# Kernel optimization log

Measured on AMD Instinct MI355X. Metric: run time of the kernel, lower is better.

The kernel has to match this reference:

```python
import jax, jax.numpy as jnp
import numpy as np

# --- APPM / NMS pipeline constants (3 ratio groups on the 28x28 mixed feature map) ---
RATIOS = [4, 6, 8]            # square sliding-window sizes in feature cells
N_LIST = [2, 3, 2]            # proposals kept per group (proposalN = 7)
IOU_THRESHS = [0.25, 0.25, 0.25]
FM_SIZE = 28                  # mixed feature map spatial size
STRIDE = 16                   # 448 / 28: feature cell -> image pixels
IMG = 448
PROPOSAL_N = sum(N_LIST)
GROUP_SIZES = [(FM_SIZE - r + 1) ** 2 for r in RATIOS]


def make_coordinates():
    """[x0, y0, x1, y1] image-space boxes for every sliding window, all groups concatenated."""
    coords = []
    for r in RATIOS:
        n = FM_SIZE - r + 1
        ii, jj = np.meshgrid(np.arange(n), np.arange(n), indexing='ij')
        x0 = (ii.ravel() * STRIDE).astype(np.int32)
        y0 = (jj.ravel() * STRIDE).astype(np.int32)
        coords.append(np.stack([x0, y0, x0 + r * STRIDE, y0 + r * STRIDE], axis=1))
    return np.concatenate(coords, axis=0).astype(np.int32)   # (1595, 4)


def window_scores_from_fm(fm):
    """AvgPool2d(r, stride=1) then sum over channels == reduce_window over channel-summed map."""
    s = jnp.sum(fm, axis=1)  # (B, H, W)
    outs = []
    for r in RATIOS:
        w = jax.lax.reduce_window(s, 0.0, jax.lax.add, (1, r, r), (1, 1, 1), 'VALID') / float(r * r)
        outs.append(w.reshape(s.shape[0], -1))
    return jnp.concatenate(outs, axis=1)  # (B, sum(GROUP_SIZES))


def nms_group(scores, boxes, n_sel, thresh):
    """Greedy IoU NMS, exactly the inclusive (+1) box math of the source nms()."""
    areas = (boxes[:, 2] - boxes[:, 0] + 1.0) * (boxes[:, 3] - boxes[:, 1] + 1.0)

    def body(k, carry):
        sc, idxs = carry
        i = jnp.argmax(sc)                       # highest remaining score
        idxs = idxs.at[k].set(i.astype(jnp.int32))
        b = boxes[i]
        xx0 = jnp.maximum(boxes[:, 0], b[0]); yy0 = jnp.maximum(boxes[:, 1], b[1])
        xx1 = jnp.minimum(boxes[:, 2], b[2]); yy1 = jnp.minimum(boxes[:, 3], b[3])
        w = xx1 - xx0 + 1.0; h = yy1 - yy0 + 1.0
        inter = jnp.where((w < 0) | (h < 0), 0.0, w * h)
        iou = inter / (areas + areas[i] - inter)
        sc = jnp.where(iou > thresh, -jnp.inf, sc)  # suppress (selected box has iou=1 -> removed)
        return sc, idxs

    _, idxs = jax.lax.fori_loop(0, n_sel, body, (scores, jnp.zeros((n_sel,), jnp.int32)))
    return idxs


def select_proposals(all_scores, coordinates):
    parts = []
    off = 0
    for ng, n_sel, th in zip(GROUP_SIZES, N_LIST, IOU_THRESHS):
        sc = all_scores[:, off:off + ng]
        bx = coordinates[off:off + ng].astype(jnp.float32)
        idx = jax.vmap(lambda s: nms_group(s, bx, n_sel, th))(sc) + off
        parts.append(idx)
        off += ng
    return jnp.concatenate(parts, axis=1)  # (B, PROPOSAL_N) global window indices


def crop_windows(x, coordinates, indices):
    """Gather-crop each proposal window from the raw image, bilinear-resize to 448x448."""
    outs = []
    col = 0
    for r, n_sel in zip(RATIOS, N_LIST):
        w = r * STRIDE  # fixed crop size for this ratio group
        idx_g = indices[:, col:col + n_sel]

        def crop_one(img, gi):
            c = coordinates[gi]
            patch = jax.lax.dynamic_slice(img, (0, c[0], c[1]), (3, w, w))
            return jax.image.resize(patch, (3, IMG, IMG), 'bilinear')

        crops = jax.vmap(lambda img, gis: jax.vmap(lambda gi: crop_one(img, gi))(gis))(x, idx_g)
        outs.append(crops)
        col += n_sel
    return jnp.concatenate(outs, axis=1)  # (B, PROPOSAL_N, 3, 448, 448)


def setup_inputs() -> dict:
    key = jax.random.key(0)
    k1, k2, k3, k4 = jax.random.split(key, 4)
    B = 8
    return {
        'x': jax.random.normal(k1, (B, 3, IMG, IMG), jnp.float32),
        'fm': jax.random.normal(k2, (B, 384, FM_SIZE, FM_SIZE), jnp.float32),
        'embedding': jax.random.normal(k3, (B, 2048), jnp.float32),
        'W_cls': jax.random.normal(k4, (2048, 200), jnp.float32) * 0.02,
        'b_cls': jnp.zeros((200,), jnp.float32),
        'coordinates': jnp.asarray(make_coordinates()),
    }


def reference(x, fm, embedding, W_cls, b_cls, coordinates):
    all_scores = window_scores_from_fm(fm)                              # window_scores (B, 1595)
    proposalN_indices = select_proposals(all_scores, coordinates)       # (B, 7) int32
    proposalN_windows_scores = jnp.take_along_axis(all_scores, proposalN_indices, axis=1)
    window_imgs = crop_windows(x, coordinates, proposalN_indices)
    window_imgs = window_imgs.reshape(-1, 3, IMG, IMG)                  # (B*7, 3, 448, 448)
    raw_logits = embedding @ W_cls + b_cls                              # rawcls_net
    return (proposalN_indices, proposalN_windows_scores, all_scores, window_imgs, raw_logits)
```

## Files before the change

kernel.cpp:

```cpp
#include <hip/hip_runtime.h>
#include <math.h>

#define THREADS 256

typedef float f32x4 __attribute__((ext_vector_type(4)));

__global__ __launch_bounds__(THREADS) void fused1_kernel(const float* __restrict__ fm,
                                                         float4* __restrict__ part,
                                                         int cpc, int K,
                                                         const float* __restrict__ emb,
                                                         const float* __restrict__ W,
                                                         float* __restrict__ lpart) {
    int blk = blockIdx.x;
    int t = threadIdx.x;
    if (blk < 8 * K) {
        int b = blk / K, k = blk - b * K;
        if (t >= 196) return;
        const float4* f = (const float4*)(fm + ((size_t)b * 384 + (size_t)k * cpc) * 784);
        float4 acc = {0.0f, 0.0f, 0.0f, 0.0f};
        for (int c = 0; c < cpc; ++c) {
            float4 v = f[(size_t)c * 196 + t];
            acc.x += v.x; acc.y += v.y; acc.z += v.z; acc.w += v.w;
        }
        part[((size_t)b * K + k) * 196 + t] = acc;
    } else {
        int idx = blk - 8 * K;
        int b = idx >> 4, kc = idx & 15;
        if (t >= 200) return;
        const float* e  = emb + (size_t)b * 2048 + kc * 128;
        const float* wp = W + (size_t)kc * 128 * 200 + t;
        float acc = 0.0f;
        #pragma unroll 4
        for (int k = 0; k < 128; ++k)
            acc += e[k] * wp[(size_t)k * 200];
        lpart[((size_t)b * 16 + kc) * 200 + t] = acc;
    }
}

__global__ __launch_bounds__(THREADS) void fused2_kernel(const float4* __restrict__ part,
                                                         int K,
                                                         float* __restrict__ all_scores,
                                                         float* __restrict__ out_idx_f,
                                                         float* __restrict__ out_sc,
                                                         int* __restrict__ ws_idx,
                                                         const float* __restrict__ lpart,
                                                         const float* __restrict__ bias,
                                                         float* __restrict__ logits) {
    __shared__ float4 s4[196];
    __shared__ float  pref[28][29];
    __shared__ float  scl[625];
    __shared__ float  rv[4];
    __shared__ int    ri[4];
    int t = threadIdx.x;

    if (blockIdx.x >= 24) {
        int b = blockIdx.x - 24;
        if (t >= 200) return;
        float acc = bias[t];
        #pragma unroll
        for (int kc = 0; kc < 16; ++kc)
            acc += lpart[((size_t)b * 16 + kc) * 200 + t];
        logits[b * 200 + t] = acc;
        return;
    }

    int b = blockIdx.x / 3, g = blockIdx.x - b * 3;

    if (t < 196) {
        float4 acc = {0.0f, 0.0f, 0.0f, 0.0f};
        #pragma unroll 8
        for (int k = 0; k < K; ++k) {
            float4 v = part[((size_t)b * K + k) * 196 + t];
            acc.x += v.x; acc.y += v.y; acc.z += v.z; acc.w += v.w;
        }
        s4[t] = acc;
    }
    __syncthreads();
    if (t < 28) {
        float4 row[7];
        #pragma unroll
        for (int i = 0; i < 7; ++i) row[i] = s4[t * 7 + i];
        float run = 0.0f;
        pref[t][0] = 0.0f;
        #pragma unroll
        for (int j = 0; j < 28; ++j) {
            run += ((float*)row)[j];
            pref[t][j + 1] = run;
        }
    }
    __syncthreads();

    const int gnA[3]   = {625, 529, 441};
    const int sideA[3] = {25, 23, 21};
    const int rA[3]    = {4, 6, 8};
    const int nselA[3] = {2, 3, 2};
    const int colA[3]  = {0, 2, 5};
    const int goffA[3] = {0, 625, 1154};

    int n = gnA[g], side = sideA[g], r = rA[g];
    int nsel = nselA[g], goff = goffA[g], colbase = colA[g];
    float inv = 1.0f / (float)(r * r);

    for (int loc = t; loc < n; loc += THREADS) {
        int i = loc / side, j = loc % side;
        float acc = 0.0f;
        for (int a = 0; a < r; ++a)
            acc += pref[i + a][j + r] - pref[i + a][j];
        float sv = acc * inv;
        scl[loc] = sv;
        all_scores[b * 1595 + goff + loc] = sv;
    }
    __syncthreads();

    float ext = (float)(r * 16 + 1);
    float A   = ext * ext;
    float rs  = (float)(r * 16);

    for (int k = 0; k < nsel; ++k) {
        float bv = -INFINITY; int bi = 0x7fffffff;
        for (int i = t; i < n; i += THREADS) {
            float v = scl[i];
            if (v > bv || (v == bv && i < bi)) { bv = v; bi = i; }
        }
        #pragma unroll
        for (int m = 1; m < 64; m <<= 1) {
            float ov = __shfl_xor(bv, m, 64);
            int   oi = __shfl_xor(bi, m, 64);
            if (ov > bv || (ov == bv && oi < bi)) { bv = ov; bi = oi; }
        }
        int wv = t >> 6;
        if ((t & 63) == 0) { rv[wv] = bv; ri[wv] = bi; }
        __syncthreads();
        if (t == 0) {
            for (int q = 1; q < 4; ++q) {
                float ov = rv[q]; int oi = ri[q];
                if (ov > bv || (ov == bv && oi < bi)) { bv = ov; bi = oi; }
            }
            ri[0] = bi;
            int outp = b * 7 + colbase + k;
            out_idx_f[outp] = (float)(goff + bi);
            out_sc[outp]    = bv;
            ws_idx[outp]    = goff + bi;
        }
        __syncthreads();
        int sel = ri[0];
        int si = sel / side, sj = sel % side;
        float sx0 = si * 16.0f, sy0 = sj * 16.0f;
        float sx1 = sx0 + rs,   sy1 = sy0 + rs;
        for (int i = t; i < n; i += THREADS) {
            int ii = i / side, jj = i % side;
            float x0 = ii * 16.0f, y0 = jj * 16.0f;
            float x1 = x0 + rs,    y1 = y0 + rs;
            float xx0 = fmaxf(x0, sx0), yy0 = fmaxf(y0, sy0);
            float xx1 = fminf(x1, sx1), yy1 = fminf(y1, sy1);
            float w = xx1 - xx0 + 1.0f, h = yy1 - yy0 + 1.0f;
            float inter = (w < 0.0f || h < 0.0f) ? 0.0f : w * h;
            float iou = inter / (A + A - inter);
            if (iou > 0.25f) scl[i] = -INFINITY;
        }
        __syncthreads();
    }
}

#define CROP_GRID 1024
#define NTASK (56 * 3 * 28)

__global__ __launch_bounds__(448) void crop_kernel(const float* __restrict__ x,
                                                   const int* __restrict__ coords,
                                                   const int* __restrict__ ws_idx,
                                                   float* __restrict__ out) {
    __shared__ float lds[2][7 * 132];
    int t = threadIdx.x;

    int rr0 = t / 132,        xx0 = t - rr0 * 132;
    int i1  = t + 448;
    int rr1 = i1 / 132,       xx1 = i1 - rr1 * 132;
    int rr2 = 6,              xx2 = t + 104;
    int row_sub = t / 56;
    int seg     = t - row_sub * 56;
    int ox0 = seg * 8;

    int task = blockIdx.x;

    int    c_w, c_rlo, c_S;
    float  c_scale, c_wm1;
    size_t c_outb;
    const float* c_base;
    float rA, rB, rC;

    {
        int p = task / 84, rem = task - p * 84;
        int ch = rem / 28, stripe = rem - ch * 28;
        int b = p / 7, col = p - b * 7;
        int g = (col < 2) ? 0 : ((col < 5) ? 1 : 2);
        c_w = (g == 0) ? 64 : ((g == 1) ? 96 : 128);
        c_scale = (float)c_w * (1.0f / 448.0f);
        c_wm1 = (float)(c_w - 1);
        c_S = stripe * 16;
        float syb = fminf(fmaxf(((float)c_S + 0.5f) * c_scale - 0.5f, 0.0f), c_wm1);
        c_rlo = (int)syb;
        int gi = ws_idx[p];
        int c0 = coords[gi * 4 + 0];
        int c1 = coords[gi * 4 + 1];
        c_base = x + (((size_t)b * 3 + ch) * 448) * 448 + c1 + (size_t)c0 * 448;
        c_outb = (((size_t)p * 3 + ch) * 448) * 448;
        rA = c_base[(size_t)min(c_rlo + rr0, c_w - 1) * 448 + min(xx0, c_w - 1)];
        rB = c_base[(size_t)min(c_rlo + rr1, c_w - 1) * 448 + min(xx1, c_w - 1)];
        if (t < 28)
            rC = c_base[(size_t)min(c_rlo + rr2, c_w - 1) * 448 + min(xx2, c_w - 1)];
    }

    int buf = 0;
    while (true) {
        lds[buf][t]       = rA;
        lds[buf][t + 448] = rB;
        if (t < 28) lds[buf][t + 896] = rC;

        int nxt = task + CROP_GRID;
        bool has_nxt = nxt < NTASK;
        int    n_w = 0, n_rlo = 0, n_S = 0;
        float  n_scale = 0.0f, n_wm1 = 0.0f;
        size_t n_outb = 0;
        const float* n_base = nullptr;
        float nA = 0.0f, nB = 0.0f, nC = 0.0f;
        if (has_nxt) {
            int p = nxt / 84, rem = nxt - p * 84;
            int ch = rem / 28, stripe = rem - ch * 28;
            int b = p / 7, col = p - b * 7;
            int g = (col < 2) ? 0 : ((col < 5) ? 1 : 2);
            n_w = (g == 0) ? 64 : ((g == 1) ? 96 : 128);
            n_scale = (float)n_w * (1.0f / 448.0f);
            n_wm1 = (float)(n_w - 1);
            n_S = stripe * 16;
            float syb = fminf(fmaxf(((float)n_S + 0.5f) * n_scale - 0.5f, 0.0f), n_wm1);
            n_rlo = (int)syb;
            int gi = ws_idx[p];
            int c0 = coords[gi * 4 + 0];
            int c1 = coords[gi * 4 + 1];
            n_base = x + (((size_t)b * 3 + ch) * 448) * 448 + c1 + (size_t)c0 * 448;
            n_outb = (((size_t)p * 3 + ch) * 448) * 448;
            nA = n_base[(size_t)min(n_rlo + rr0, n_w - 1) * 448 + min(xx0, n_w - 1)];
            nB = n_base[(size_t)min(n_rlo + rr1, n_w - 1) * 448 + min(xx1, n_w - 1)];
            if (t < 28)
                nC = n_base[(size_t)min(n_rlo + rr2, n_w - 1) * 448 + min(xx2, n_w - 1)];
        }

        __syncthreads();

        {
            float sxb = ((float)ox0 + 0.5f) * c_scale - 0.5f;
            float sxc = fminf(fmaxf(sxb, 0.0f), c_wm1);
            int   i0  = (int)sxc;
            int   dk[8];
            float txk[8];
            #pragma unroll
            for (int k = 0; k < 8; ++k) {
                float sx = fminf(fmaxf(sxb + (float)k * c_scale, 0.0f), c_wm1);
                int xi = (int)sx;
                dk[k]  = xi - i0;
                txk[k] = sx - (float)xi;
            }
            const float* lbase = &lds[buf][0];
            #pragma unroll
            for (int half = 0; half < 2; ++half) {
                int oy = c_S + half * 8 + row_sub;
                float sy = fminf(fmaxf(((float)oy + 0.5f) * c_scale - 0.5f, 0.0f), c_wm1);
                int   y0 = (int)sy;
                int   y1 = min(y0 + 1, c_w - 1);
                float ty = sy - (float)y0;
                const float* l0 = lbase + (y0 - c_rlo) * 132 + i0;
                const float* l1 = lbase + (y1 - c_rlo) * 132 + i0;
                float a0 = l0[0], a1 = l0[1], a2 = l0[2], a3 = l0[3];
                float b0 = l1[0], b1 = l1[1], b2 = l1[2], b3 = l1[3];

                f32x4 res0, res1;
                #pragma unroll
                for (int k = 0; k < 8; ++k) {
                    int   d   = dk[k];
                    float v00 = (d == 0) ? a0 : ((d == 1) ? a1 : a2);
                    float v01 = (d == 0) ? a1 : ((d == 1) ? a2 : a3);
                    float v10 = (d == 0) ? b0 : ((d == 1) ? b1 : b2);
                    float v11 = (d == 0) ? b1 : ((d == 1) ? b2 : b3);
                    float tx  = txk[k];
                    float top = v00 + tx * (v01 - v00);
                    float bot = v10 + tx * (v11 - v10);
                    float rr  = top + ty * (bot - top);
                    if (k < 4) res0[k] = rr; else res1[k - 4] = rr;
                }
                float* orow = out + c_outb + (size_t)oy * 448 + ox0;
                *(f32x4*)orow       = res0;
                *(f32x4*)(orow + 4) = res1;
            }
        }

        if (!has_nxt) break;
        c_w = n_w; c_rlo = n_rlo; c_S = n_S;
        c_scale = n_scale; c_wm1 = n_wm1;
        c_outb = n_outb; c_base = n_base;
        rA = nA; rB = nB; rC = nC;
        task = nxt;
        buf ^= 1;
    }
}

extern "C" void kernel_launch(void* const* d_in, const int* in_sizes, int n_in,
                              void* d_out, int out_size, void* d_ws, size_t ws_size,
                              hipStream_t stream) {
    const float* x      = (const float*)d_in[0];
    const float* fm     = (const float*)d_in[1];
    const float* emb    = (const float*)d_in[2];
    const float* Wc     = (const float*)d_in[3];
    const float* bc     = (const float*)d_in[4];
    const int*   coords = (const int*)d_in[5];

    float* out        = (float*)d_out;
    float* out_idx    = out;
    float* out_sc     = out + 56;
    float* all_scores = out + 112;
    float* imgs       = out + 12872;
    float* logits     = out + 33731144;

    int K = 32;
    while (K > 1 && ws_size < 1024 + (size_t)8 * K * 784 * 4 + 25600 * 4) K >>= 1;
    int cpc = 384 / K;

    int*    ws_idx = (int*)d_ws;
    float4* part   = (float4*)((char*)d_ws + 1024);
    float*  lpart  = (float*)((char*)d_ws + 1024 + (size_t)8 * K * 784 * 4);

    fused1_kernel<<<8 * K + 128, THREADS, 0, stream>>>(fm, part, cpc, K, emb, Wc, lpart);
    fused2_kernel<<<32, THREADS, 0, stream>>>(part, K, all_scores, out_idx, out_sc, ws_idx,
                                              lpart, bc, logits);
    crop_kernel<<<CROP_GRID, 448, 0, stream>>>(x, coords, ws_idx, imgs);
}
```

Measured before the change: 53.12 us.

## Precompute crop source offsets and overlap next-task loads with resize compute

The selection kernel now writes a per-proposal pixel offset into the source image, so the crop kernel no longer does a dependent ws_idx→coords lookup chain. In the crop loop, the LDS store and a lightweight barrier come before the next task's global loads, which are issued after the barrier so they are in flight during the current bilinear compute. The interpolation select is rewritten as precomputed differences plus fmaf, and the persistent grid changes from 1024 to 944 blocks. The main risks are correctness of the hand-written barrier ordering and uneven load balance from the new grid size.

```diff
diff --git a/kernel.cpp b/kernel.cpp
--- a/kernel.cpp
+++ b/kernel.cpp
@@ -2,6 +2,8 @@
 #include <math.h>
 
 #define THREADS 256
+#define CROP_GRID 944
+#define NTASK (56 * 3 * 28)
 
 typedef float f32x4 __attribute__((ext_vector_type(4)));
 
@@ -43,6 +45,8 @@
                                                          float* __restrict__ out_idx_f,
                                                          float* __restrict__ out_sc,
                                                          int* __restrict__ ws_idx,
+                                                         int* __restrict__ soff,
+                                                         const int* __restrict__ coords,
                                                          const float* __restrict__ lpart,
                                                          const float* __restrict__ bias,
                                                          float* __restrict__ logits) {
@@ -138,9 +142,11 @@
             }
             ri[0] = bi;
             int outp = b * 7 + colbase + k;
-            out_idx_f[outp] = (float)(goff + bi);
+            int gi   = goff + bi;
+            out_idx_f[outp] = (float)gi;
             out_sc[outp]    = bv;
-            ws_idx[outp]    = goff + bi;
+            ws_idx[outp]    = gi;
+            soff[outp]      = coords[gi * 4 + 0] * 448 + coords[gi * 4 + 1];
         }
         __syncthreads();
         int sel = ri[0];
@@ -162,142 +168,131 @@
     }
 }
 
-#define CROP_GRID 1024
-#define NTASK (56 * 3 * 28)
-
 __global__ __launch_bounds__(448) void crop_kernel(const float* __restrict__ x,
-                                                   const int* __restrict__ coords,
-                                                   const int* __restrict__ ws_idx,
+                                                   const int* __restrict__ soff,
                                                    float* __restrict__ out) {
-    __shared__ float lds[2][7 * 132];
+    __shared__ float lds[2][924];
     int t = threadIdx.x;
 
-    int rr0 = t / 132,        xx0 = t - rr0 * 132;
+    int rr0 = t / 132, xx0 = t - rr0 * 132;
     int i1  = t + 448;
-    int rr1 = i1 / 132,       xx1 = i1 - rr1 * 132;
-    int rr2 = 6,              xx2 = t + 104;
+    int rr1 = i1 / 132, xx1 = i1 - rr1 * 132;
+    int xx2 = t + 104;
     int row_sub = t / 56;
     int seg     = t - row_sub * 56;
     int ox0 = seg * 8;
 
     int task = blockIdx.x;
-
-    int    c_w, c_rlo, c_S;
-    float  c_scale, c_wm1;
-    size_t c_outb;
-    const float* c_base;
-    float rA, rB, rC;
-
+    int cw; float cscale, cwm1; int cS, crlo; float* coutb;
+    float rA, rB, rC = 0.0f;
     {
         int p = task / 84, rem = task - p * 84;
         int ch = rem / 28, stripe = rem - ch * 28;
         int b = p / 7, col = p - b * 7;
         int g = (col < 2) ? 0 : ((col < 5) ? 1 : 2);
-        c_w = (g == 0) ? 64 : ((g == 1) ? 96 : 128);
-        c_scale = (float)c_w * (1.0f / 448.0f);
-        c_wm1 = (float)(c_w - 1);
-        c_S = stripe * 16;
-        float syb = fminf(fmaxf(((float)c_S + 0.5f) * c_scale - 0.5f, 0.0f), c_wm1);
-        c_rlo = (int)syb;
-        int gi = ws_idx[p];
-        int c0 = coords[gi * 4 + 0];
-        int c1 = coords[gi * 4 + 1];
-        c_base = x + (((size_t)b * 3 + ch) * 448) * 448 + c1 + (size_t)c0 * 448;
-        c_outb = (((size_t)p * 3 + ch) * 448) * 448;
-        rA = c_base[(size_t)min(c_rlo + rr0, c_w - 1) * 448 + min(xx0, c_w - 1)];
-        rB = c_base[(size_t)min(c_rlo + rr1, c_w - 1) * 448 + min(xx1, c_w - 1)];
+        cw = (g == 0) ? 64 : ((g == 1) ? 96 : 128);
+        cscale = (float)cw * (1.0f / 448.0f);
+        cwm1 = (float)(cw - 1);
+        cS = stripe * 16;
+        float syb = fminf(fmaxf(((float)cS + 0.5f) * cscale - 0.5f, 0.0f), cwm1);
+        crlo = (int)syb;
+        const float* cbase = x + ((size_t)(b * 3 + ch)) * 200704 + soff[p];
+        coutb = out + ((size_t)(p * 3 + ch)) * 200704;
+        rA = cbase[(size_t)min(crlo + rr0, cw - 1) * 448 + min(xx0, cw - 1)];
+        rB = cbase[(size_t)min(crlo + rr1, cw - 1) * 448 + min(xx1, cw - 1)];
         if (t < 28)
-            rC = c_base[(size_t)min(c_rlo + rr2, c_w - 1) * 448 + min(xx2, c_w - 1)];
+            rC = cbase[(size_t)min(crlo + 6, cw - 1) * 448 + min(xx2, cw - 1)];
     }
 
     int buf = 0;
     while (true) {
-        lds[buf][t]       = rA;
-        lds[buf][t + 448] = rB;
-        if (t < 28) lds[buf][t + 896] = rC;
-
         int nxt = task + CROP_GRID;
-        bool has_nxt = nxt < NTASK;
-        int    n_w = 0, n_rlo = 0, n_S = 0;
-        float  n_scale = 0.0f, n_wm1 = 0.0f;
-        size_t n_outb = 0;
-        const float* n_base = nullptr;
-        float nA = 0.0f, nB = 0.0f, nC = 0.0f;
-        if (has_nxt) {
+        bool has = nxt < NTASK;
+
+        int nw = 0, nrlo = 0, nS = 0, nso = 0, nb3 = 0, np3 = 0;
+        float nscale = 0.0f, nwm1 = 0.0f;
+        if (has) {
             int p = nxt / 84, rem = nxt - p * 84;
             int ch = rem / 28, stripe = rem - ch * 28;
             int b = p / 7, col = p - b * 7;
             int g = (col < 2) ? 0 : ((col < 5) ? 1 : 2);
-            n_w = (g == 0) ? 64 : ((g == 1) ? 96 : 128);
-            n_scale = (float)n_w * (1.0f / 448.0f);
-            n_wm1 = (float)(n_w - 1);
-            n_S = stripe * 16;
-            float syb = fminf(fmaxf(((float)n_S + 0.5f) * n_scale - 0.5f, 0.0f), n_wm1);
-            n_rlo = (int)syb;
-            int gi = ws_idx[p];
-            int c0 = coords[gi * 4 + 0];
-            int c1 = coords[gi * 4 + 1];
-            n_base = x + (((size_t)b * 3 + ch) * 448) * 448 + c1 + (size_t)c0 * 448;
-            n_outb = (((size_t)p * 3 + ch) * 448) * 448;
-            nA = n_base[(size_t)min(n_rlo + rr0, n_w - 1) * 448 + min(xx0, n_w - 1)];
-            nB = n_base[(size_t)min(n_rlo + rr1, n_w - 1) * 448 + min(xx1, n_w - 1)];
+            nw = (g == 0) ? 64 : ((g == 1) ? 96 : 128);
+            nscale = (float)nw * (1.0f / 448.0f);
+            nwm1 = (float)(nw - 1);
+            nS = stripe * 16;
+            float syb = fminf(fmaxf(((float)nS + 0.5f) * nscale - 0.5f, 0.0f), nwm1);
+            nrlo = (int)syb;
+            nso = soff[p];
+            nb3 = b * 3 + ch;
+            np3 = p * 3 + ch;
+        }
+
+        lds[buf][t]       = rA;
+        lds[buf][t + 448] = rB;
+        if (t < 28) lds[buf][t + 896] = rC;
+        asm volatile("s_waitcnt lgkmcnt(0)" ::: "memory");
+        __builtin_amdgcn_s_barrier();
+
+        float* noutb = nullptr;
+        if (has) {
+            const float* nbase = x + (size_t)nb3 * 200704 + nso;
+            noutb = out + (size_t)np3 * 200704;
+            rA = nbase[(size_t)min(nrlo + rr0, nw - 1) * 448 + min(xx0, nw - 1)];
+            rB = nbase[(size_t)min(nrlo + rr1, nw - 1) * 448 + min(xx1, nw - 1)];
             if (t < 28)
-                nC = n_base[(size_t)min(n_rlo + rr2, n_w - 1) * 448 + min(xx2, n_w - 1)];
-        }
-
-        __syncthreads();
+                rC = nbase[(size_t)min(nrlo + 6, nw - 1) * 448 + min(xx2, nw - 1)];
+        }
 
         {
-            float sxb = ((float)ox0 + 0.5f) * c_scale - 0.5f;
-            float sxc = fminf(fmaxf(sxb, 0.0f), c_wm1);
+            float sxb = ((float)ox0 + 0.5f) * cscale - 0.5f;
+            float sxc = fminf(fmaxf(sxb, 0.0f), cwm1);
             int   i0  = (int)sxc;
-            int   dk[8];
             float txk[8];
+            bool  e1[8], e2[8];
             #pragma unroll
             for (int k = 0; k < 8; ++k) {
-                float sx = fminf(fmaxf(sxb + (float)k * c_scale, 0.0f), c_wm1);
+                float sx = fminf(fmaxf(sxb + (float)k * cscale, 0.0f), cwm1);
                 int xi = (int)sx;
-                dk[k]  = xi - i0;
                 txk[k] = sx - (float)xi;
+                int d  = xi - i0;
+                e1[k] = (d >= 1);
+                e2[k] = (d >= 2);
             }
             const float* lbase = &lds[buf][0];
             #pragma unroll
             for (int half = 0; half < 2; ++half) {
-                int oy = c_S + half * 8 + row_sub;
-                float sy = fminf(fmaxf(((float)oy + 0.5f) * c_scale - 0.5f, 0.0f), c_wm1);
+                int oy = cS + half * 8 + row_sub;
+                float sy = fminf(fmaxf(((float)oy + 0.5f) * cscale - 0.5f, 0.0f), cwm1);
                 int   y0 = (int)sy;
-                int   y1 = min(y0 + 1, c_w - 1);
+                int   y1 = min(y0 + 1, cw - 1);
                 float ty = sy - (float)y0;
-                const float* l0 = lbase + (y0 - c_rlo) * 132 + i0;
-                const float* l1 = lbase + (y1 - c_rlo) * 132 + i0;
+                const float* l0 = lbase + (y0 - crlo) * 132 + i0;
+                const float* l1 = lbase + (y1 - crlo) * 132 + i0;
                 float a0 = l0[0], a1 = l0[1], a2 = l0[2], a3 = l0[3];
                 float b0 = l1[0], b1 = l1[1], b2 = l1[2], b3 = l1[3];
+                float da0 = a1 - a0, da1 = a2 - a1, da2 = a3 - a2;
+                float db0 = b1 - b0, db1 = b2 - b1, db2 = b3 - b2;
 
                 f32x4 res0, res1;
                 #pragma unroll
                 for (int k = 0; k < 8; ++k) {
-                    int   d   = dk[k];
-                    float v00 = (d == 0) ? a0 : ((d == 1) ? a1 : a2);
-                    float v01 = (d == 0) ? a1 : ((d == 1) ? a2 : a3);
-                    float v10 = (d == 0) ? b0 : ((d == 1) ? b1 : b2);
-                    float v11 = (d == 0) ? b1 : ((d == 1) ? b2 : b3);
-                    float tx  = txk[k];
-                    float top = v00 + tx * (v01 - v00);
-                    float bot = v10 + tx * (v11 - v10);
+                    float av  = e2[k] ? a2  : (e1[k] ? a1  : a0);
+                    float dav = e2[k] ? da2 : (e1[k] ? da1 : da0);
+                    float bv  = e2[k] ? b2  : (e1[k] ? b1  : b0);
+                    float dbv = e2[k] ? db2 : (e1[k] ? db1 : db0);
+                    float top = fmaf(txk[k], dav, av);
+                    float bot = fmaf(txk[k], dbv, bv);
                     float rr  = top + ty * (bot - top);
                     if (k < 4) res0[k] = rr; else res1[k - 4] = rr;
                 }
-                float* orow = out + c_outb + (size_t)oy * 448 + ox0;
+                float* orow = coutb + (size_t)oy * 448 + ox0;
                 *(f32x4*)orow       = res0;
                 *(f32x4*)(orow + 4) = res1;
             }
         }
 
-        if (!has_nxt) break;
-        c_w = n_w; c_rlo = n_rlo; c_S = n_S;
-        c_scale = n_scale; c_wm1 = n_wm1;
-        c_outb = n_outb; c_base = n_base;
-        rA = nA; rB = nB; rC = nC;
+        if (!has) break;
+        cw = nw; cscale = nscale; cwm1 = nwm1; cS = nS; crlo = nrlo; coutb = noutb;
         task = nxt;
         buf ^= 1;
     }
@@ -325,11 +320,12 @@
     int cpc = 384 / K;
 
     int*    ws_idx = (int*)d_ws;
+    int*    soff   = (int*)((char*)d_ws + 256);
     float4* part   = (float4*)((char*)d_ws + 1024);
     float*  lpart  = (float*)((char*)d_ws + 1024 + (size_t)8 * K * 784 * 4);
 
     fused1_kernel<<<8 * K + 128, THREADS, 0, stream>>>(fm, part, cpc, K, emb, Wc, lpart);
     fused2_kernel<<<32, THREADS, 0, stream>>>(part, K, all_scores, out_idx, out_sc, ws_idx,
-                                              lpart, bc, logits);
-    crop_kernel<<<CROP_GRID, 448, 0, stream>>>(x, coords, ws_idx, imgs);
+                                              soff, coords, lpart, bc, logits);
+    crop_kernel<<<CROP_GRID, 448, 0, stream>>>(x, soff, imgs);
 }
```

Measured after the change: 54.25 us. +2.1%, slower.
